# Optimization experiments

Hardware: AMD Instinct MI355X
Metric: run time of the kernel (lower is better)

## Reference

```python
import jax, jax.numpy as jnp
import numpy as np

N_ATOMS = 100_000
N_EDGES = 1_600_000
N_RADIAL = 16
N_ELEM = 119          # periodic table size used by per-element scale/shift
HIDDEN = 512
N_FEAT = N_RADIAL + N_RADIAL * N_RADIAL  # M0 + M1-contraction features = 272
R_CUT = 5.0
EPS = 1e-8


def setup_inputs() -> dict:
    key = jax.random.key(0)
    ks = jax.random.split(key, 10)
    R = jax.random.normal(ks[0], (N_ATOMS, 3), jnp.float32)
    Z = jax.random.randint(ks[1], (N_ATOMS,), 0, N_ELEM).astype(jnp.int32)
    idx = jax.random.randint(ks[2], (2, N_EDGES), 0, N_ATOMS)
    box = jnp.zeros((3, 3), jnp.float32)
    offsets = jnp.zeros((N_EDGES, 3), jnp.float32)
    # descriptor params: Gaussian radial basis centers / width
    centers = jnp.linspace(0.0, R_CUT, N_RADIAL, dtype=jnp.float32)
    width = jnp.asarray(0.5, jnp.float32)
    # readout MLP params
    W1 = jax.random.normal(ks[3], (N_FEAT, HIDDEN), jnp.float32) / np.sqrt(N_FEAT)
    b1 = jnp.zeros((HIDDEN,), jnp.float32)
    W2 = jax.random.normal(ks[4], (HIDDEN, HIDDEN), jnp.float32) / np.sqrt(HIDDEN)
    b2 = jnp.zeros((HIDDEN,), jnp.float32)
    W3 = jax.random.normal(ks[5], (HIDDEN, 1), jnp.float32) / np.sqrt(HIDDEN)
    b3 = jnp.zeros((1,), jnp.float32)
    # per-element scale/shift
    scale = jnp.ones((N_ELEM,), jnp.float32)
    shift = jax.random.normal(ks[6], (N_ELEM,), jnp.float32)
    return {"R": R, "Z": Z, "idx": idx, "box": box, "offsets": offsets,
            "centers": centers, "width": width,
            "W1": W1, "b1": b1, "W2": W2, "b2": b2, "W3": W3, "b3": b3,
            "scale": scale, "shift": shift}


def reference(R, Z, idx, box, offsets, centers, width,
              W1, b1, W2, b2, W3, b3, scale, shift):
    n = R.shape[0]
    idx_i, idx_j = idx[0], idx[1]
    # edge gather + free displacement (init_box == 0): dr = displacement(Rj, Ri) = Rj - Ri
    dr = R[idx_j] - R[idx_i]                      # (E, 3)
    r = jnp.linalg.norm(dr, axis=-1, keepdims=True)  # (E, 1)
    d = dr / (r + EPS)                            # unit directions (E, 3)
    # Gaussian radial basis (E, K)
    b = jnp.exp(-((r - centers[None, :]) ** 2) / (2.0 * width * width))
    # scatter-sum moments per atom
    M0 = jax.ops.segment_sum(b, idx_i, num_segments=n)                       # (N, K)
    M1 = jax.ops.segment_sum(b[:, :, None] * d[:, None, :], idx_i,
                             num_segments=n)                                 # (N, K, 3)
    # rotation-invariant gaussian-moment contraction
    G1 = jnp.einsum('nad,nbd->nab', M1, M1).reshape(n, -1)                   # (N, K*K)
    feat = jnp.concatenate([M0, G1], axis=-1)                                # (N, 272)
    # per-atom readout MLP (swish)
    h = jax.nn.silu(feat @ W1 + b1)
    h = jax.nn.silu(h @ W2 + b2)
    h = h @ W3 + b3                                                          # (N, 1)
    # per-element scale/shift, then total energy
    atomic_energies = scale[Z][:, None] * h + shift[Z][:, None]
    return jnp.sum(atomic_energies)
```

## Files before the change

kernel.cpp:

```cpp
#include <hip/hip_runtime.h>
#include <hip/hip_bf16.h>
#include <cstdint>

#define HID 512
#define K1P 288
#define K1F 160

typedef __attribute__((ext_vector_type(8))) short bf16x8;
typedef __attribute__((ext_vector_type(4))) float f32x4;

__device__ __forceinline__ short f2bf(float x) {
    __hip_bfloat16 h = __float2bfloat16(x);
    return *(short*)&h;
}
__device__ __forceinline__ float silu(float x) {
    return x * (1.0f / (1.0f + __expf(-x)));
}
__device__ __forceinline__ void gl_lds16(const void* src, void* dst) {
    __builtin_amdgcn_global_load_lds(
        (const __attribute__((address_space(1))) void*)src,
        (__attribute__((address_space(3))) void*)dst, 16, 0, 0);
}
__device__ __forceinline__ int xcd_swz(int bid, int nwg) {
    int q = nwg >> 3, r = nwg & 7;
    int xcd = bid & 7, i = bid >> 3;
    int base = (xcd < r) ? xcd * (q + 1) : r * (q + 1) + (xcd - r) * q;
    return base + i;
}
__device__ __forceinline__ void tri_ab(int g, int& a, int& b) {
    int aa = 0, rem = g;
    while (rem >= 16 - aa) { rem -= 16 - aa; ++aa; }
    a = aa; b = aa + rem;
}

__global__ __launch_bounds__(256) void hist_kernel(
    const int* __restrict__ idx, int* __restrict__ counts, int nEdges)
{
    int e = blockIdx.x * 256 + threadIdx.x;
    if (e < nEdges) atomicAdd(&counts[idx[e]], 1);
}

__global__ __launch_bounds__(1024) void scan1_kernel(
    const int* __restrict__ counts, int* __restrict__ starts,
    int* __restrict__ blockSum, int n)
{
    __shared__ int wsum[16];
    int t = threadIdx.x, lane = t & 63, wid = t >> 6;
    int i = blockIdx.x * 1024 + t;
    int v = (i < n) ? counts[i] : 0;
    int incl = v;
    #pragma unroll
    for (int off = 1; off < 64; off <<= 1) {
        int u = __shfl_up(incl, off);
        if (lane >= off) incl += u;
    }
    if (lane == 63) wsum[wid] = incl;
    __syncthreads();
    if (t < 16) {
        int s = wsum[t];
        #pragma unroll
        for (int off = 1; off < 16; off <<= 1) {
            int u = __shfl_up(s, off);
            if (t >= off) s += u;
        }
        wsum[t] = s;
    }
    __syncthreads();
    int woff = (wid == 0) ? 0 : wsum[wid - 1];
    if (i < n) starts[i] = woff + incl - v;
    if (t == 0) blockSum[blockIdx.x] = wsum[15];
}

__global__ __launch_bounds__(1024) void scan2_kernel(
    const int* __restrict__ blockSum, int* __restrict__ blockOff,
    int* __restrict__ starts, int nb, int n)
{
    __shared__ int arr[1024];
    int t = threadIdx.x;
    int v = (t < nb) ? blockSum[t] : 0;
    arr[t] = v;
    __syncthreads();
    #pragma unroll
    for (int off = 1; off < 1024; off <<= 1) {
        int x = (t >= off) ? arr[t - off] : 0;
        __syncthreads();
        arr[t] += x;
        __syncthreads();
    }
    if (t < nb) blockOff[t] = arr[t] - v;
    if (t == 0) starts[n] = arr[nb - 1];
}

__global__ __launch_bounds__(1024) void scan3_kernel(
    int* __restrict__ starts, int* __restrict__ cursor,
    const int* __restrict__ blockOff, int n)
{
    int i = blockIdx.x * 1024 + threadIdx.x;
    if (i < n) {
        int s = starts[i] + blockOff[blockIdx.x];
        starts[i] = s;
        cursor[i] = s;
    }
}

__global__ __launch_bounds__(256) void scatter_kernel(
    const float* __restrict__ R, const int* __restrict__ idx,
    int* __restrict__ cursor, float4* __restrict__ sorted, int nEdges)
{
    int e = blockIdx.x * 256 + threadIdx.x;
    if (e >= nEdges) return;
    int i = idx[e];
    int j = idx[nEdges + e];
    float rix = R[3*(size_t)i], riy = R[3*(size_t)i+1], riz = R[3*(size_t)i+2];
    float rjx = R[3*(size_t)j], rjy = R[3*(size_t)j+1], rjz = R[3*(size_t)j+2];
    float dx = rjx - rix, dy = rjy - riy, dz = rjz - riz;
    float r = sqrtf(dx*dx + dy*dy + dz*dz);
    float inv = 1.0f / (r + 1e-8f);
    int pos = atomicAdd(&cursor[i], 1);
    sorted[pos] = make_float4(r, dx*inv, dy*inv, dz*inv);
}

__global__ __launch_bounds__(256) void accum_kernel(
    const float4* __restrict__ sorted, const int* __restrict__ starts,
    const float* __restrict__ centers, const float* __restrict__ width,
    float* __restrict__ M0M1, short* __restrict__ feat16,
    int nAtoms, int useFeat)
{
    __shared__ float sm[4][64];
    int wv = threadIdx.x >> 6, lane = threadIdx.x & 63;
    int atom = blockIdx.x * 4 + wv;
    if (atom >= nAtoms) return;
    int s = starts[atom], e = starts[atom + 1];
    int k = lane >> 2, c = lane & 3;
    float ck = centers[k];
    float w = width[0];
    float inv2w2 = 1.0f / (2.0f * w * w);
    float acc = 0.0f;
    auto term = [&](float4 v) {
        float diff = v.x - ck;
        float b = __expf(-diff * diff * inv2w2);
        float comp = (c == 0) ? 1.0f : ((c == 1) ? v.y : ((c == 2) ? v.z : v.w));
        return b * comp;
    };
    int p = s;
    for (; p + 3 < e; p += 4) {
        float4 v0 = sorted[p];
        float4 v1 = sorted[p + 1];
        float4 v2 = sorted[p + 2];
        float4 v3 = sorted[p + 3];
        acc += term(v0); acc += term(v1); acc += term(v2); acc += term(v3);
    }
    for (; p < e; ++p) acc += term(sorted[p]);

    if (!useFeat) {
        M0M1[(size_t)atom * 64 + lane] = acc;
        return;
    }
    sm[wv][lane] = acc;
    asm volatile("s_waitcnt lgkmcnt(0)" ::: "memory");
    short* frow = feat16 + (size_t)atom * K1F;
    #pragma unroll
    for (int q = 0; q < 3; ++q) {
        int idx5 = q * 64 + lane;
        if (idx5 >= K1F) break;
        float val;
        if (idx5 < 16) {
            val = sm[wv][4 * idx5];
        } else if (idx5 < 152) {
            int a, b;
            tri_ab(idx5 - 16, a, b);
            val = sm[wv][4*a+1] * sm[wv][4*b+1]
                + sm[wv][4*a+2] * sm[wv][4*b+2]
                + sm[wv][4*a+3] * sm[wv][4*b+3];
        } else {
            val = 0.0f;
        }
        frow[idx5] = f2bf(val);
    }
}

__global__ __launch_bounds__(256) void convW_kernel(
    const float* __restrict__ W, short* __restrict__ Wt, int K, int Kpad, int N)
{
    int n = blockIdx.x * 256 + threadIdx.x;
    int k = blockIdx.y;
    if (n >= N) return;
    float v = (k < K) ? W[(size_t)k * N + n] : 0.0f;
    Wt[(size_t)n * Kpad + k] = f2bf(v);
}

__global__ __launch_bounds__(256) void convW1f_kernel(
    const float* __restrict__ W, short* __restrict__ Wf, int N)
{
    int n = blockIdx.x * 256 + threadIdx.x;
    int k = blockIdx.y;
    if (n >= N) return;
    float v;
    if (k < 16) {
        v = W[(size_t)k * N + n];
    } else if (k < 152) {
        int a, b;
        tri_ab(k - 16, a, b);
        v = W[(size_t)(16 + a*16 + b) * N + n];
        if (b > a) v += W[(size_t)(16 + b*16 + a) * N + n];
    } else {
        v = 0.0f;
    }
    Wf[(size_t)n * K1F + k] = f2bf(v);
}

__global__ __launch_bounds__(256, 2) void gemm1_mfma(
    const float* __restrict__ M0M1, const short* __restrict__ W1t,
    const float* __restrict__ bias, short* __restrict__ C, int M, int nwg)
{
    __shared__ float MsT[64][128];
    __shared__ short Asl[2][4096];
    __shared__ short Bsl[4][4096];
    int t = threadIdx.x;
    int w = t >> 6, lane = t & 63;
    int wr = w >> 1, wc = w & 1;
    int li = lane & 15, lg = lane >> 4;
    int lin = xcd_swz(blockIdx.x, nwg);
    int row0 = (lin >> 2) * 128;
    int col0 = (lin & 3) * 128;

    {
        int mrow = t >> 1, mo = (t & 1) * 32;
        int gm = row0 + mrow; if (gm > M - 1) gm = M - 1;
        const float4* src = (const float4*)(M0M1 + (size_t)gm * 64 + mo);
        #pragma unroll
        for (int q = 0; q < 8; ++q) {
            float4 v = src[q];
            int c0 = mo + q * 4;
            MsT[c0+0][mrow] = v.x; MsT[c0+1][mrow] = v.y;
            MsT[c0+2][mrow] = v.z; MsT[c0+3][mrow] = v.w;
        }
    }
    __syncthreads();

    auto stageA = [&](int kt, int buf) {
        #pragma unroll
        for (int p = 0; p < 2; ++p) {
            int cell = p * 256 + t;
            int k8 = cell >> 7, row = cell & 127;
            int kbase = kt * 32 + k8 * 8;
            bf16x8 v;
            if (kbase < 16) {
                #pragma unroll
                for (int j = 0; j < 8; ++j) v[j] = f2bf(MsT[4*(kbase+j)][row]);
            } else if (kbase < 272) {
                int g = kbase - 16, a = g >> 4, b0 = g & 15;
                float ax = MsT[4*a+1][row], ay = MsT[4*a+2][row], az = MsT[4*a+3][row];
                #pragma unroll
                for (int j = 0; j < 8; ++j) {
                    int b = b0 + j;
                    v[j] = f2bf(ax*MsT[4*b+1][row] + ay*MsT[4*b+2][row] + az*MsT[4*b+3][row]);
                }
            } else {
                #pragma unroll
                for (int j = 0; j < 8; ++j) v[j] = 0;
            }
            *(bf16x8*)&Asl[buf][cell * 8] = v;
        }
    };
    auto stageB = [&](int kt, int buf) {
        #pragma unroll
        for (int p = 0; p < 2; ++p) {
            int cell = p * 256 + t;
            int k8 = cell >> 7, col = cell & 127;
            const short* src = W1t + (size_t)(col0 + col) * K1P + kt*32 + k8*8;
            gl_lds16(src, &Bsl[buf][(p * 256 + w * 64) * 8]);
        }
    };

    f32x4 acc[4][4] = {};
    const int NS = K1P / 32;
    stageA(0, 0);
    stageB(0, 0); stageB(1, 1); stageB(2, 2);

    #pragma unroll
    for (int s = 0; s < NS; ++s) {
        if (s <= NS - 3)      asm volatile("s_waitcnt vmcnt(4) lgkmcnt(0)\n\ts_barrier" ::: "memory");
        else if (s == NS - 2) asm volatile("s_waitcnt vmcnt(2) lgkmcnt(0)\n\ts_barrier" ::: "memory");
        else                  asm volatile("s_waitcnt vmcnt(0) lgkmcnt(0)\n\ts_barrier" ::: "memory");
        if (s + 3 < NS) stageB(s + 3, (s + 3) & 3);
        bf16x8 af[4], bfr[4];
        #pragma unroll
        for (int m = 0; m < 4; ++m)
            af[m] = *(const bf16x8*)&Asl[s & 1][(lg*128 + wr*64 + m*16 + li) * 8];
        #pragma unroll
        for (int n = 0; n < 4; ++n)
            bfr[n] = *(const bf16x8*)&Bsl[s & 3][(lg*128 + wc*64 + n*16 + li) * 8];
        if (s + 1 < NS) stageA(s + 1, (s + 1) & 1);
        __builtin_amdgcn_s_setprio(1);
        #pragma unroll
        for (int m = 0; m < 4; ++m)
            #pragma unroll
            for (int n = 0; n < 4; ++n)
                acc[m][n] = __builtin_amdgcn_mfma_f32_16x16x32_bf16(af[m], bfr[n], acc[m][n], 0, 0, 0);
        __builtin_amdgcn_s_setprio(0);
    }

    float bv[4];
    #pragma unroll
    for (int n = 0; n < 4; ++n) bv[n] = bias[col0 + wc*64 + n*16 + li];
    #pragma unroll
    for (int m = 0; m < 4; ++m)
        #pragma unroll
        for (int r = 0; r < 4; ++r) {
            int row = row0 + wr*64 + m*16 + lg*4 + r;
            if (row >= M) continue;
            size_t base = (size_t)row * HID + col0 + wc*64 + li;
            #pragma unroll
            for (int n = 0; n < 4; ++n) {
                float cx = acc[m][n][r] + bv[n];
                C[base + n*16] = f2bf(silu(cx));
            }
        }
}

__global__ __launch_bounds__(256, 3) void gemm_feat(
    const short* __restrict__ F, const short* __restrict__ W1f,
    const float* __restrict__ bias, short* __restrict__ C, int M, int nwg)
{
    __shared__ short Asl[3][4096];
    __shared__ short Bsl[3][4096];
    int t = threadIdx.x;
    int w = t >> 6, lane = t & 63;
    int wr = w >> 1, wc = w & 1;
    int li = lane & 15, lg = lane >> 4;
    int lin = xcd_swz(blockIdx.x, nwg);
    int row0 = (lin >> 2) * 128;
    int col0 = (lin & 3) * 128;

    int rr = t & 127, k8h = t >> 7;
    int grA = row0 + rr; if (grA > M - 1) grA = M - 1;
    const short* aSrc0 = F + (size_t)grA * K1F + k8h * 8;
    const short* aSrc1 = aSrc0 + 16;
    const short* bSrc0 = W1f + (size_t)(col0 + rr) * K1F + k8h * 8;
    const short* bSrc1 = bSrc0 + 16;

    auto stage = [&](int kt, int buf) {
        gl_lds16(aSrc0 + kt * 32, &Asl[buf][(w * 64) * 8]);
        gl_lds16(aSrc1 + kt * 32, &Asl[buf][(256 + w * 64) * 8]);
        gl_lds16(bSrc0 + kt * 32, &Bsl[buf][(w * 64) * 8]);
        gl_lds16(bSrc1 + kt * 32, &Bsl[buf][(256 + w * 64) * 8]);
    };

    f32x4 acc[4][4] = {};
    const int NS = K1F / 32;
    stage(0, 0); stage(1, 1);

    #pragma unroll
    for (int s = 0; s < NS; ++s) {
        if (s < NS - 1) asm volatile("s_waitcnt vmcnt(4)\n\ts_barrier" ::: "memory");
        else            asm volatile("s_waitcnt vmcnt(0)\n\ts_barrier" ::: "memory");
        if (s + 2 < NS) stage(s + 2, (s + 2) % 3);
        bf16x8 af[4], bfr[4];
        #pragma unroll
        for (int m = 0; m < 4; ++m)
            af[m] = *(const bf16x8*)&Asl[s % 3][(lg*128 + wr*64 + m*16 + li) * 8];
        #pragma unroll
        for (int n = 0; n < 4; ++n)
            bfr[n] = *(const bf16x8*)&Bsl[s % 3][(lg*128 + wc*64 + n*16 + li) * 8];
        __builtin_amdgcn_s_setprio(1);
        #pragma unroll
        for (int m = 0; m < 4; ++m)
            #pragma unroll
            for (int n = 0; n < 4; ++n)
                acc[m][n] = __builtin_amdgcn_mfma_f32_16x16x32_bf16(af[m], bfr[n], acc[m][n], 0, 0, 0);
        __builtin_amdgcn_s_setprio(0);
    }

    float bv[4];
    #pragma unroll
    for (int n = 0; n < 4; ++n) bv[n] = bias[col0 + wc*64 + n*16 + li];
    #pragma unroll
    for (int m = 0; m < 4; ++m)
        #pragma unroll
        for (int r = 0; r < 4; ++r) {
            int row = row0 + wr*64 + m*16 + lg*4 + r;
            if (row >= M) continue;
            size_t base = (size_t)row * HID + col0 + wc*64 + li;
            #pragma unroll
            for (int n = 0; n < 4; ++n) {
                float cx = acc[m][n][r] + bv[n];
                C[base + n*16] = f2bf(silu(cx));
            }
        }
}

__global__ __launch_bounds__(256, 3) void gemm2_mfma(
    const short* __restrict__ A, const short* __restrict__ W2t,
    const float* __restrict__ bias, const float* __restrict__ W3,
    const float* __restrict__ b3, const float* __restrict__ scale,
    const float* __restrict__ shift, const int* __restrict__ Z,
    float* __restrict__ out, int M, int nwg)
{
    __shared__ short Asl[3][4096];
    __shared__ short Bsl[3][4096];
    __shared__ float rsum[2][128];
    __shared__ float red[4];
    int t = threadIdx.x;
    int w = t >> 6, lane = t & 63;
    int wr = w >> 1, wc = w & 1;
    int li = lane & 15, lg = lane >> 4;
    int lin = xcd_swz(blockIdx.x, nwg);
    int row0 = (lin >> 2) * 128;
    int col0 = (lin & 3) * 128;

    int rr = t & 127, k8h = t >> 7;
    int grA = row0 + rr; if (grA > M - 1) grA = M - 1;
    const short* aSrc0 = A + (size_t)grA * HID + k8h * 8;
    const short* aSrc1 = aSrc0 + 16;
    const short* bSrc0 = W2t + (size_t)(col0 + rr) * HID + k8h * 8;
    const short* bSrc1 = bSrc0 + 16;

    auto stage = [&](int kt, int buf) {
        gl_lds16(aSrc0 + kt * 32, &Asl[buf][(w * 64) * 8]);
        gl_lds16(aSrc1 + kt * 32, &Asl[buf][(256 + w * 64) * 8]);
        gl_lds16(bSrc0 + kt * 32, &Bsl[buf][(w * 64) * 8]);
        gl_lds16(bSrc1 + kt * 32, &Bsl[buf][(256 + w * 64) * 8]);
    };

    f32x4 acc[4][4] = {};
    const int NS = HID / 32;
    stage(0, 0); stage(1, 1);

    for (int s = 0; s < NS; ++s) {
        if (s < NS - 1) asm volatile("s_waitcnt vmcnt(4)\n\ts_barrier" ::: "memory");
        else            asm volatile("s_waitcnt vmcnt(0)\n\ts_barrier" ::: "memory");
        if (s + 2 < NS) stage(s + 2, (s + 2) % 3);
        bf16x8 af[4], bfr[4];
        #pragma unroll
        for (int m = 0; m < 4; ++m)
            af[m] = *(const bf16x8*)&Asl[s % 3][(lg*128 + wr*64 + m*16 + li) * 8];
        #pragma unroll
        for (int n = 0; n < 4; ++n)
            bfr[n] = *(const bf16x8*)&Bsl[s % 3][(lg*128 + wc*64 + n*16 + li) * 8];
        __builtin_amdgcn_s_setprio(1);
        #pragma unroll
        for (int m = 0; m < 4; ++m)
            #pragma unroll
            for (int n = 0; n < 4; ++n)
                acc[m][n] = __builtin_amdgcn_mfma_f32_16x16x32_bf16(af[m], bfr[n], acc[m][n], 0, 0, 0);
        __builtin_amdgcn_s_setprio(0);
    }

    float bv[4], w3v[4];
    #pragma unroll
    for (int n = 0; n < 4; ++n) {
        int col = col0 + wc*64 + n*16 + li;
        bv[n]  = bias[col];
        w3v[n] = W3[col];
    }
    #pragma unroll
    for (int m = 0; m < 4; ++m)
        #pragma unroll
        for (int r = 0; r < 4; ++r) {
            float s = 0.f;
            #pragma unroll
            for (int n = 0; n < 4; ++n) {
                float cx = acc[m][n][r] + bv[n];
                s += silu(cx) * w3v[n];
            }
            #pragma unroll
            for (int off = 1; off < 16; off <<= 1) s += __shfl_xor(s, off);
            if (li == 0) rsum[wc][wr*64 + m*16 + lg*4 + r] = s;
        }
    __syncthreads();
    float e = 0.f;
    if (t < 128) {
        int row = row0 + t;
        if (row < M) {
            float v = rsum[0][t] + rsum[1][t];
            int z = Z[row];
            e = scale[z] * v;
            if ((lin & 3) == 0) e += scale[z] * b3[0] + shift[z];
        }
    }
    #pragma unroll
    for (int off = 32; off > 0; off >>= 1) e += __shfl_down(e, off);
    if (lane == 0) red[w] = e;
    __syncthreads();
    if (t == 0) atomicAdd(out, red[0] + red[1] + red[2] + red[3]);
}

extern "C" void kernel_launch(void* const* d_in, const int* in_sizes, int n_in,
                              void* d_out, int out_size, void* d_ws, size_t ws_size,
                              hipStream_t stream)
{
    const float* R       = (const float*)d_in[0];
    const int*   Z       = (const int*)  d_in[1];
    const int*   idx     = (const int*)  d_in[2];
    const float* centers = (const float*)d_in[5];
    const float* width   = (const float*)d_in[6];
    const float* W1      = (const float*)d_in[7];
    const float* b1      = (const float*)d_in[8];
    const float* W2      = (const float*)d_in[9];
    const float* b2      = (const float*)d_in[10];
    const float* W3      = (const float*)d_in[11];
    const float* b3      = (const float*)d_in[12];
    const float* scale   = (const float*)d_in[13];
    const float* shift   = (const float*)d_in[14];

    int nAtoms = in_sizes[0] / 3;
    int nEdges = in_sizes[2] / 2;

    size_t m0m1_b = (size_t)nAtoms * 64 * sizeof(float);
    size_t h1_b   = (size_t)nAtoms * HID * 2;
    size_t w1t_b  = (size_t)HID * K1P * 2;
    size_t w2t_b  = (size_t)HID * HID * 2;
    size_t w1f_b  = (size_t)HID * K1F * 2;
    size_t feat_b = (size_t)nAtoms * K1F * 2;
    if (ws_size < m0m1_b + h1_b + w1t_b + w2t_b) return;
    int useFeat = (ws_size >= m0m1_b + h1_b + w1t_b + w2t_b + w1f_b + feat_b) ? 1 : 0;

    char* ws = (char*)d_ws;
    float* M0M1  = (float*)ws;
    char*  regB  = ws + m0m1_b;
    short* h1    = (short*)regB;
    short* W1t   = (short*)(ws + m0m1_b + h1_b);
    short* W2t   = W1t + (size_t)HID * K1P;
    short* W1f   = W2t + (size_t)HID * HID;
    short* feat16 = (short*)(ws + m0m1_b + h1_b + w1t_b + w2t_b + w1f_b);

    int nb = (nAtoms + 1023) / 1024;
    size_t sorted_b = (size_t)nEdges * sizeof(float4);
    float4* sorted = (float4*)regB;
    int* counts   = (int*)(regB + sorted_b);
    int* starts   = counts + nAtoms;
    int* cursor   = starts + nAtoms + 1;
    int* blockSum = cursor + nAtoms;
    int* blockOff = blockSum + nb;
    if (sorted_b + (size_t)(3 * nAtoms + 1 + 2 * nb) * sizeof(int) > h1_b) return;

    float* out = (float*)d_out;

    hipMemsetAsync(counts, 0, (size_t)nAtoms * sizeof(int), stream);
    hipMemsetAsync(out, 0, sizeof(float), stream);

    convW_kernel<<<dim3(2, K1P), 256, 0, stream>>>(W1, W1t, 272, K1P, HID);
    convW_kernel<<<dim3(2, HID), 256, 0, stream>>>(W2, W2t, HID, HID, HID);
    if (useFeat)
        convW1f_kernel<<<dim3(2, K1F), 256, 0, stream>>>(W1, W1f, HID);

    int eb = (nEdges + 255) / 256;
    hist_kernel <<<eb, 256, 0, stream>>>(idx, counts, nEdges);
    scan1_kernel<<<nb, 1024, 0, stream>>>(counts, starts, blockSum, nAtoms);
    scan2_kernel<<<1, 1024, 0, stream>>>(blockSum, blockOff, starts, nb, nAtoms);
    scan3_kernel<<<nb, 1024, 0, stream>>>(starts, cursor, blockOff, nAtoms);
    scatter_kernel<<<eb, 256, 0, stream>>>(R, idx, cursor, sorted, nEdges);
    accum_kernel<<<(nAtoms + 3) / 4, 256, 0, stream>>>(sorted, starts, centers, width,
                                                       M0M1, feat16, nAtoms, useFeat);

    int gb = (nAtoms + 127) / 128;
    int nwg = gb * 4;
    if (useFeat)
        gemm_feat<<<nwg, 256, 0, stream>>>(feat16, W1f, b1, h1, nAtoms, nwg);
    else
        gemm1_mfma<<<nwg, 256, 0, stream>>>(M0M1, W1t, b1, h1, nAtoms, nwg);
    gemm2_mfma<<<nwg, 256, 0, stream>>>(h1, W2t, b2, W3, b3, scale, shift, Z, out, nAtoms, nwg);
}
```

Before: 426.7 us.

## Scatter neighbor indices only and compute edge geometry in accumulation kernel

The scatter kernel now writes only the neighbor index j (4 bytes) into the CSR-sorted buffer instead of a precomputed float4 (r, unit vector), and no longer gathers positions. The accumulation kernel loads each atom's own position once, has each lane fetch one neighbor's position and compute distance and direction, then broadcasts these across the wave with shuffles. This cuts the scattered write and sequential read traffic by about 4x and drops R gathers for atom i in the scatter. In exchange it adds a random R gather in accum and a serial shuffle loop per edge.

```diff
diff --git a/kernel.cpp b/kernel.cpp
--- a/kernel.cpp
+++ b/kernel.cpp
@@ -104,24 +104,20 @@
 }
 
 __global__ __launch_bounds__(256) void scatter_kernel(
-    const float* __restrict__ R, const int* __restrict__ idx,
-    int* __restrict__ cursor, float4* __restrict__ sorted, int nEdges)
+    const int* __restrict__ idx, int* __restrict__ cursor,
+    int* __restrict__ jsorted, int nEdges)
 {
     int e = blockIdx.x * 256 + threadIdx.x;
     if (e >= nEdges) return;
     int i = idx[e];
     int j = idx[nEdges + e];
-    float rix = R[3*(size_t)i], riy = R[3*(size_t)i+1], riz = R[3*(size_t)i+2];
-    float rjx = R[3*(size_t)j], rjy = R[3*(size_t)j+1], rjz = R[3*(size_t)j+2];
-    float dx = rjx - rix, dy = rjy - riy, dz = rjz - riz;
-    float r = sqrtf(dx*dx + dy*dy + dz*dz);
-    float inv = 1.0f / (r + 1e-8f);
     int pos = atomicAdd(&cursor[i], 1);
-    sorted[pos] = make_float4(r, dx*inv, dy*inv, dz*inv);
+    jsorted[pos] = j;
 }
 
 __global__ __launch_bounds__(256) void accum_kernel(
-    const float4* __restrict__ sorted, const int* __restrict__ starts,
+    const float* __restrict__ R, const int* __restrict__ jsorted,
+    const int* __restrict__ starts,
     const float* __restrict__ centers, const float* __restrict__ width,
     float* __restrict__ M0M1, short* __restrict__ feat16,
     int nAtoms, int useFeat)
@@ -135,22 +131,31 @@
     float ck = centers[k];
     float w = width[0];
     float inv2w2 = 1.0f / (2.0f * w * w);
+    float rix = R[3*(size_t)atom], riy = R[3*(size_t)atom+1], riz = R[3*(size_t)atom+2];
+
     float acc = 0.0f;
-    auto term = [&](float4 v) {
-        float diff = v.x - ck;
-        float b = __expf(-diff * diff * inv2w2);
-        float comp = (c == 0) ? 1.0f : ((c == 1) ? v.y : ((c == 2) ? v.z : v.w));
-        return b * comp;
-    };
-    int p = s;
-    for (; p + 3 < e; p += 4) {
-        float4 v0 = sorted[p];
-        float4 v1 = sorted[p + 1];
-        float4 v2 = sorted[p + 2];
-        float4 v3 = sorted[p + 3];
-        acc += term(v0); acc += term(v1); acc += term(v2); acc += term(v3);
-    }
-    for (; p < e; ++p) acc += term(sorted[p]);
+    for (int p = s; p < e; p += 64) {
+        int cnt = e - p; if (cnt > 64) cnt = 64;
+        float er = 0.f, eux = 0.f, euy = 0.f, euz = 0.f;
+        if (lane < cnt) {
+            int j = jsorted[p + lane];
+            float jx = R[3*(size_t)j], jy = R[3*(size_t)j+1], jz = R[3*(size_t)j+2];
+            float dx = jx - rix, dy = jy - riy, dz = jz - riz;
+            float rr = sqrtf(dx*dx + dy*dy + dz*dz);
+            float inv = 1.0f / (rr + 1e-8f);
+            er = rr; eux = dx*inv; euy = dy*inv; euz = dz*inv;
+        }
+        for (int q = 0; q < cnt; ++q) {
+            float rq  = __shfl(er,  q);
+            float uxq = __shfl(eux, q);
+            float uyq = __shfl(euy, q);
+            float uzq = __shfl(euz, q);
+            float diff = rq - ck;
+            float b = __expf(-diff * diff * inv2w2);
+            float comp = (c == 0) ? 1.0f : ((c == 1) ? uxq : ((c == 2) ? uyq : uzq));
+            acc += b * comp;
+        }
+    }
 
     if (!useFeat) {
         M0M1[(size_t)atom * 64 + lane] = acc;
@@ -526,14 +531,14 @@
     short* feat16 = (short*)(ws + m0m1_b + h1_b + w1t_b + w2t_b + w1f_b);
 
     int nb = (nAtoms + 1023) / 1024;
-    size_t sorted_b = (size_t)nEdges * sizeof(float4);
-    float4* sorted = (float4*)regB;
-    int* counts   = (int*)(regB + sorted_b);
+    size_t jsort_b = (size_t)nEdges * sizeof(int);
+    int* jsorted  = (int*)regB;
+    int* counts   = (int*)(regB + jsort_b);
     int* starts   = counts + nAtoms;
     int* cursor   = starts + nAtoms + 1;
     int* blockSum = cursor + nAtoms;
     int* blockOff = blockSum + nb;
-    if (sorted_b + (size_t)(3 * nAtoms + 1 + 2 * nb) * sizeof(int) > h1_b) return;
+    if (jsort_b + (size_t)(3 * nAtoms + 1 + 2 * nb) * sizeof(int) > h1_b) return;
 
     float* out = (float*)d_out;
 
@@ -550,8 +555,8 @@
     scan1_kernel<<<nb, 1024, 0, stream>>>(counts, starts, blockSum, nAtoms);
     scan2_kernel<<<1, 1024, 0, stream>>>(blockSum, blockOff, starts, nb, nAtoms);
     scan3_kernel<<<nb, 1024, 0, stream>>>(starts, cursor, blockOff, nAtoms);
-    scatter_kernel<<<eb, 256, 0, stream>>>(R, idx, cursor, sorted, nEdges);
-    accum_kernel<<<(nAtoms + 3) / 4, 256, 0, stream>>>(sorted, starts, centers, width,
+    scatter_kernel<<<eb, 256, 0, stream>>>(idx, cursor, jsorted, nEdges);
+    accum_kernel<<<(nAtoms + 3) / 4, 256, 0, stream>>>(R, jsorted, starts, centers, width,
                                                        M0M1, feat16, nAtoms, useFeat);
 
     int gb = (nAtoms + 127) / 128;
```

Result: slower. 469.0 us (+9.9%).

## Partition edge scatter by destination atom range per XCD group

Applied to the files above, without the earlier changes.

Replaces the one-thread-per-edge scatter with a grid of 8 groups of 96 blocks. Each group reads every edge with vectorized int4 loads but only writes edges whose source atom falls in its eighth of the atom range. Block index mod 8 selects the group, so each group lines up with one XCD and its atomics and sorted writes stay within that XCD's L2. The cost is reading the edge index list eight times and looping over many more edges per thread.

```diff
diff --git a/kernel.cpp b/kernel.cpp
--- a/kernel.cpp
+++ b/kernel.cpp
@@ -5,6 +5,7 @@
 #define HID 512
 #define K1P 288
 #define K1F 160
+#define NBG 96
 
 typedef __attribute__((ext_vector_type(8))) short bf16x8;
 typedef __attribute__((ext_vector_type(4))) float f32x4;
@@ -103,21 +104,40 @@
     }
 }
 
-__global__ __launch_bounds__(256) void scatter_kernel(
+__global__ __launch_bounds__(256) void scatter2_kernel(
     const float* __restrict__ R, const int* __restrict__ idx,
-    int* __restrict__ cursor, float4* __restrict__ sorted, int nEdges)
-{
-    int e = blockIdx.x * 256 + threadIdx.x;
-    if (e >= nEdges) return;
-    int i = idx[e];
-    int j = idx[nEdges + e];
-    float rix = R[3*(size_t)i], riy = R[3*(size_t)i+1], riz = R[3*(size_t)i+2];
-    float rjx = R[3*(size_t)j], rjy = R[3*(size_t)j+1], rjz = R[3*(size_t)j+2];
-    float dx = rjx - rix, dy = rjy - riy, dz = rjz - riz;
-    float r = sqrtf(dx*dx + dy*dy + dz*dz);
-    float inv = 1.0f / (r + 1e-8f);
-    int pos = atomicAdd(&cursor[i], 1);
-    sorted[pos] = make_float4(r, dx*inv, dy*inv, dz*inv);
+    int* __restrict__ cursor, float4* __restrict__ sorted, int nEdges, int nAtoms)
+{
+    int g  = blockIdx.x & 7;
+    int gb = blockIdx.x >> 3;
+    int per = (nAtoms + 7) >> 3;
+    int lo = g * per;
+    int hi = lo + per; if (hi > nAtoms) hi = nAtoms;
+
+    auto emit = [&](int i, int j) {
+        if (i < lo || i >= hi) return;
+        float rix = R[3*(size_t)i], riy = R[3*(size_t)i+1], riz = R[3*(size_t)i+2];
+        float rjx = R[3*(size_t)j], rjy = R[3*(size_t)j+1], rjz = R[3*(size_t)j+2];
+        float dx = rjx - rix, dy = rjy - riy, dz = rjz - riz;
+        float r = sqrtf(dx*dx + dy*dy + dz*dz);
+        float inv = 1.0f / (r + 1e-8f);
+        int pos = atomicAdd(&cursor[i], 1);
+        sorted[pos] = make_float4(r, dx*inv, dy*inv, dz*inv);
+    };
+
+    if ((nEdges & 3) == 0) {
+        int nq = nEdges >> 2;
+        const int4* i4p = (const int4*)idx;
+        const int4* j4p = (const int4*)(idx + nEdges);
+        for (int q = gb * 256 + threadIdx.x; q < nq; q += NBG * 256) {
+            int4 iv = i4p[q], jv = j4p[q];
+            emit(iv.x, jv.x); emit(iv.y, jv.y);
+            emit(iv.z, jv.z); emit(iv.w, jv.w);
+        }
+    } else {
+        for (int e = gb * 256 + threadIdx.x; e < nEdges; e += NBG * 256)
+            emit(idx[e], idx[nEdges + e]);
+    }
 }
 
 __global__ __launch_bounds__(256) void accum_kernel(
@@ -550,7 +570,7 @@
     scan1_kernel<<<nb, 1024, 0, stream>>>(counts, starts, blockSum, nAtoms);
     scan2_kernel<<<1, 1024, 0, stream>>>(blockSum, blockOff, starts, nb, nAtoms);
     scan3_kernel<<<nb, 1024, 0, stream>>>(starts, cursor, blockOff, nAtoms);
-    scatter_kernel<<<eb, 256, 0, stream>>>(R, idx, cursor, sorted, nEdges);
+    scatter2_kernel<<<8 * NBG, 256, 0, stream>>>(R, idx, cursor, sorted, nEdges, nAtoms);
     accum_kernel<<<(nAtoms + 3) / 4, 256, 0, stream>>>(sorted, starts, centers, width,
                                                        M0M1, feat16, nAtoms, useFeat);
 
```

Result: no change. 423.3 us (-0.8%).
